# Performance work log

Hardware: AMD Instinct MI355X
Metric: run time of the kernel (lower is better)

## Reference

```python
import jax, jax.numpy as jnp
import numpy as np

N_NODES = 50000
N_EDGES = 800000
D = 128


def setup_inputs() -> dict:
    key = jax.random.key(0)
    ks = jax.random.split(key, 8)
    scale = 1.0 / np.sqrt(D)
    x = jax.random.normal(ks[0], (N_NODES, D), dtype=jnp.float32)
    edge_index = jax.random.randint(ks[1], (2, N_EDGES), 0, N_NODES, dtype=jnp.int64)
    return {
        "x": x,
        "edge_index": edge_index,
        "w1_l": jax.random.normal(ks[2], (D, D), dtype=jnp.float32) * scale,
        "w1_r": jax.random.normal(ks[3], (D, D), dtype=jnp.float32) * scale,
        "b1": jnp.zeros((D,), dtype=jnp.float32),
        "w2_l": jax.random.normal(ks[4], (D, D), dtype=jnp.float32) * scale,
        "w2_r": jax.random.normal(ks[5], (D, D), dtype=jnp.float32) * scale,
        "b2": jnp.zeros((D,), dtype=jnp.float32),
    }


def _sage_conv(x, src, dst, w_l, w_r, b):
    # mean aggregation of source features at destination nodes
    n = x.shape[0]
    msg = x[src]                                            # [E, D] gather
    agg = jax.ops.segment_sum(msg, dst, num_segments=n)      # [N, D] scatter-add
    cnt = jax.ops.segment_sum(jnp.ones((src.shape[0],), x.dtype), dst, num_segments=n)
    mean = agg / jnp.maximum(cnt, 1.0)[:, None]
    # out = lin_l(mean_agg) + lin_r(x) + bias  (PyG SAGEConv default)
    return mean @ w_l.T + x @ w_r.T + b


def reference(x, edge_index, w1_l, w1_r, b1, w2_l, w2_r, b2):
    src, dst = edge_index[0], edge_index[1]
    h = jax.nn.relu(_sage_conv(x, src, dst, w1_l, w1_r, b1))
    out = _sage_conv(h, src, dst, w2_l, w2_r, b2)
    return out
```

## Files before the change

### kernel.cpp

```cpp
#include <hip/hip_runtime.h>

#define D 128
#define CAP 48

typedef unsigned short u16;
typedef unsigned int u32;
typedef __attribute__((ext_vector_type(8))) short short8;
typedef __attribute__((ext_vector_type(4))) float f32x4;
typedef __attribute__((ext_vector_type(4))) unsigned short us4;
typedef __attribute__((ext_vector_type(8))) unsigned short us8;

__device__ __forceinline__ float bf2f(u16 v) {
    union { u32 u; float f; } c; c.u = ((u32)v) << 16; return c.f;
}
__device__ __forceinline__ u16 f2bf(float f) {
    union { float f; u32 u; } c; c.f = f;
    u32 r = (c.u + 0x7FFFu + ((c.u >> 16) & 1u)) >> 16;
    return (u16)r;
}

__global__ __launch_bounds__(256) void prep_kernel(const float* __restrict__ x,
                                                   u16* __restrict__ xb, int n8,
                                                   const float* __restrict__ w1l,
                                                   const float* __restrict__ w1r,
                                                   const float* __restrict__ w2l,
                                                   const float* __restrict__ w2r,
                                                   u16* __restrict__ wb1,
                                                   u16* __restrict__ wb2,
                                                   int* __restrict__ cnt, int Nceil,
                                                   int cvtBlocks, int wBlocks) {
    const int b = blockIdx.x;
    const int t = threadIdx.x;
    if (b < cvtBlocks) {
        int i = b * 256 + t;
        if (i < n8) {
            float4 v0 = reinterpret_cast<const float4*>(x)[2 * i];
            float4 v1 = reinterpret_cast<const float4*>(x)[2 * i + 1];
            us8 o;
            o[0] = f2bf(v0.x); o[1] = f2bf(v0.y); o[2] = f2bf(v0.z); o[3] = f2bf(v0.w);
            o[4] = f2bf(v1.x); o[5] = f2bf(v1.y); o[6] = f2bf(v1.z); o[7] = f2bf(v1.w);
            reinterpret_cast<us8*>(xb)[i] = o;
        }
    } else if (b < cvtBlocks + wBlocks) {
        int e = (b - cvtBlocks) * 256 + t;
        int which = e >> 15;
        int i = e & 32767;
        int j = i >> 8, k = i & 255;
        const float* wl = which ? w2l : w1l;
        const float* wr = which ? w2r : w1r;
        u16* wb = which ? wb2 : wb1;
        float v = (k < 128) ? wl[j * 128 + k] : wr[j * 128 + k - 128];
        wb[i] = f2bf(v);
    } else {
        int i = (b - cvtBlocks - wBlocks) * 256 + t;
        if (i < Nceil) cnt[i] = 0;
    }
}

__global__ __launch_bounds__(256) void fill_pad_xcd(const int* __restrict__ src,
                                                    const int* __restrict__ dst,
                                                    int* __restrict__ cnt,
                                                    int* __restrict__ edge_pad,
                                                    int E, int bucketDiv, int perChunk) {
    const int b = blockIdx.x & 7;
    const int chunk = blockIdx.x >> 3;
    const int lo = b * bucketDiv;
    const int hi = lo + bucketDiv;
    const int beg = chunk * perChunk;
    const int end = min(E, beg + perChunk);
    for (int base = beg + threadIdx.x * 4; base < end; base += 1024) {
        if (base + 3 < end) {
            int4 d = *reinterpret_cast<const int4*>(dst + base);
            if (d.x >= lo && d.x < hi) { int p = atomicAdd(&cnt[d.x], 1); if (p < CAP) edge_pad[d.x * CAP + p] = src[base + 0]; }
            if (d.y >= lo && d.y < hi) { int p = atomicAdd(&cnt[d.y], 1); if (p < CAP) edge_pad[d.y * CAP + p] = src[base + 1]; }
            if (d.z >= lo && d.z < hi) { int p = atomicAdd(&cnt[d.z], 1); if (p < CAP) edge_pad[d.z * CAP + p] = src[base + 2]; }
            if (d.w >= lo && d.w < hi) { int p = atomicAdd(&cnt[d.w], 1); if (p < CAP) edge_pad[d.w * CAP + p] = src[base + 3]; }
        } else {
            for (int j = 0; j < 4 && base + j < end; ++j) {
                int d = dst[base + j];
                if (d >= lo && d < hi) { int p = atomicAdd(&cnt[d], 1); if (p < CAP) edge_pad[d * CAP + p] = src[base + j]; }
            }
        }
    }
}

template <int RELU, int OUTBF16>
__global__ __launch_bounds__(256) void sage_fused(const u16* __restrict__ feat,
                                                  const int* __restrict__ cnt,
                                                  const int* __restrict__ edge_pad,
                                                  const u16* __restrict__ wb,
                                                  const float* __restrict__ bias,
                                                  float* __restrict__ outf,
                                                  u16* __restrict__ outb, int n) {
    __shared__ u16 sM[32 * 128];
    __shared__ int eLds[32 * CAP];
    __shared__ int degLds[32];
    const int t = threadIdx.x;
    const int base = blockIdx.x * 32;
    char* sMb = reinterpret_cast<char*>(sM);

    {
        const int4* gseg = reinterpret_cast<const int4*>(edge_pad + (size_t)base * CAP);
#pragma unroll
        for (int i = 0; i < (32 * CAP / 4 + 255) / 256; ++i) {
            int idx = i * 256 + t;
            if (idx < 32 * CAP / 4) reinterpret_cast<int4*>(eLds)[idx] = gseg[idx];
        }
        if (t < 32) degLds[t] = (base + t < n) ? cnt[base + t] : 0;
    }
    __syncthreads();

    {
        const int halfId = t >> 5;
        const int lane = t & 31;
#pragma unroll
        for (int rnd = 0; rnd < 4; ++rnd) {
            const int nl = rnd * 8 + halfId;
            const int deg = degLds[nl];
            const int stored = min(deg, CAP);
            const int* ep = &eLds[nl * CAP];

            float a0 = 0.f, a1 = 0.f, a2 = 0.f, a3 = 0.f;
            int j = 0;
            for (; j + 8 <= stored; j += 8) {
                int4 ia = *reinterpret_cast<const int4*>(ep + j);
                int4 ib = *reinterpret_cast<const int4*>(ep + j + 4);
                us4 v0 = *reinterpret_cast<const us4*>(feat + (size_t)ia.x * D + lane * 4);
                us4 v1 = *reinterpret_cast<const us4*>(feat + (size_t)ia.y * D + lane * 4);
                us4 v2 = *reinterpret_cast<const us4*>(feat + (size_t)ia.z * D + lane * 4);
                us4 v3 = *reinterpret_cast<const us4*>(feat + (size_t)ia.w * D + lane * 4);
                us4 v4 = *reinterpret_cast<const us4*>(feat + (size_t)ib.x * D + lane * 4);
                us4 v5 = *reinterpret_cast<const us4*>(feat + (size_t)ib.y * D + lane * 4);
                us4 v6 = *reinterpret_cast<const us4*>(feat + (size_t)ib.z * D + lane * 4);
                us4 v7 = *reinterpret_cast<const us4*>(feat + (size_t)ib.w * D + lane * 4);
                a0 += (bf2f(v0[0]) + bf2f(v1[0])) + (bf2f(v2[0]) + bf2f(v3[0]))
                    + (bf2f(v4[0]) + bf2f(v5[0])) + (bf2f(v6[0]) + bf2f(v7[0]));
                a1 += (bf2f(v0[1]) + bf2f(v1[1])) + (bf2f(v2[1]) + bf2f(v3[1]))
                    + (bf2f(v4[1]) + bf2f(v5[1])) + (bf2f(v6[1]) + bf2f(v7[1]));
                a2 += (bf2f(v0[2]) + bf2f(v1[2])) + (bf2f(v2[2]) + bf2f(v3[2]))
                    + (bf2f(v4[2]) + bf2f(v5[2])) + (bf2f(v6[2]) + bf2f(v7[2]));
                a3 += (bf2f(v0[3]) + bf2f(v1[3])) + (bf2f(v2[3]) + bf2f(v3[3]))
                    + (bf2f(v4[3]) + bf2f(v5[3])) + (bf2f(v6[3]) + bf2f(v7[3]));
            }
            for (; j < stored; ++j) {
                int s = ep[j];
                us4 v = *reinterpret_cast<const us4*>(feat + (size_t)s * D + lane * 4);
                a0 += bf2f(v[0]); a1 += bf2f(v[1]); a2 += bf2f(v[2]); a3 += bf2f(v[3]);
            }

            const float sc = (deg > 0) ? (1.f / (float)deg) : 0.f;
            us4 o;
            o[0] = f2bf(a0 * sc); o[1] = f2bf(a1 * sc); o[2] = f2bf(a2 * sc); o[3] = f2bf(a3 * sc);
            int lin = nl * 256 + lane * 8;
            *reinterpret_cast<us4*>(sMb + (lin ^ ((nl & 7) << 4))) = o;
        }
    }
    __syncthreads();

    const int wid = t >> 6, lane = t & 63;
    const int l15 = lane & 15, l4 = lane >> 4;
    const int colBase = wid * 32;

    int rowA[2];
#pragma unroll
    for (int m = 0; m < 2; ++m) {
        int r = base + m * 16 + l15;
        rowA[m] = (r < n) ? r : 0;
    }

    f32x4 acc[2][2];
#pragma unroll
    for (int m = 0; m < 2; ++m)
#pragma unroll
        for (int q = 0; q < 2; ++q) acc[m][q] = (f32x4){0.f, 0.f, 0.f, 0.f};

    const int swr = (l15 & 7) << 4;

#pragma unroll
    for (int ks = 0; ks < 8; ++ks) {
        short8 afr[2];
        if (ks < 4) {
#pragma unroll
            for (int m = 0; m < 2; ++m) {
                int lin = (m * 16 + l15) * 256 + ks * 64 + l4 * 16;
                afr[m] = *reinterpret_cast<const short8*>(sMb + (lin ^ swr));
            }
        } else {
            const int kk = (ks & 3) * 32 + l4 * 8;
#pragma unroll
            for (int m = 0; m < 2; ++m)
                afr[m] = *reinterpret_cast<const short8*>(feat + (size_t)rowA[m] * D + kk);
        }
#pragma unroll
        for (int q = 0; q < 2; ++q) {
            short8 bfr = *reinterpret_cast<const short8*>(
                wb + (size_t)(colBase + q * 16 + l15) * 256 + ks * 32 + l4 * 8);
#pragma unroll
            for (int m = 0; m < 2; ++m)
                acc[m][q] = __builtin_amdgcn_mfma_f32_16x16x32_bf16(afr[m], bfr, acc[m][q], 0, 0, 0);
        }
    }

#pragma unroll
    for (int q = 0; q < 2; ++q) {
        const int col = colBase + q * 16 + l15;
        const float bv = bias[col];
#pragma unroll
        for (int m = 0; m < 2; ++m) {
#pragma unroll
            for (int r = 0; r < 4; ++r) {
                int orow = base + m * 16 + l4 * 4 + r;
                if (orow < n) {
                    float v = acc[m][q][r] + bv;
                    if (RELU) v = fmaxf(v, 0.f);
                    if (OUTBF16)
                        outb[(size_t)orow * D + col] = f2bf(v);
                    else
                        outf[(size_t)orow * D + col] = v;
                }
            }
        }
    }
}

extern "C" void kernel_launch(void* const* d_in, const int* in_sizes, int n_in,
                              void* d_out, int out_size, void* d_ws, size_t ws_size,
                              hipStream_t stream) {
    const float* x   = (const float*)d_in[0];
    const int*   ei  = (const int*)d_in[1];
    const float* w1l = (const float*)d_in[2];
    const float* w1r = (const float*)d_in[3];
    const float* b1  = (const float*)d_in[4];
    const float* w2l = (const float*)d_in[5];
    const float* w2r = (const float*)d_in[6];
    const float* b2  = (const float*)d_in[7];
    float* out = (float*)d_out;

    const int N = in_sizes[0] / D;
    const int E = in_sizes[1] / 2;

    const int* src = ei;
    const int* dst = ei + E;

    const int gridFused = (N + 31) / 32;
    const int Nceil = gridFused * 32;

    char* ws = (char*)d_ws;
    auto align = [](size_t v) { return (v + 255) & ~(size_t)255; };
    const size_t featB = align((size_t)N * D * sizeof(u16));

    u16* xb       = (u16*)ws;   ws += featB;
    u16* hb       = (u16*)ws;   ws += featB;
    u16* wb1      = (u16*)ws;   ws += align(128 * 256 * sizeof(u16));
    u16* wb2      = (u16*)ws;   ws += align(128 * 256 * sizeof(u16));
    int* cnt      = (int*)ws;   ws += align((size_t)Nceil * sizeof(int));
    int* edge_pad = (int*)ws;   ws += align((size_t)Nceil * CAP * sizeof(int));

    const int n8        = N * D / 8;
    const int cvtBlocks = (n8 + 255) / 256;
    const int wBlocks   = 256;
    const int zBlocks   = (Nceil + 255) / 256;
    const int bucketDiv = (N + 7) / 8;
    const int perChunk  = 5120;
    const int chunks    = (E + perChunk - 1) / perChunk;

    prep_kernel<<<cvtBlocks + wBlocks + zBlocks, 256, 0, stream>>>(
        x, xb, n8, w1l, w1r, w2l, w2r, wb1, wb2, cnt, Nceil, cvtBlocks, wBlocks);

    fill_pad_xcd<<<8 * chunks, 256, 0, stream>>>(src, dst, cnt, edge_pad, E, bucketDiv, perChunk);

    sage_fused<1, 1><<<gridFused, 256, 0, stream>>>(xb, cnt, edge_pad, wb1, b1, nullptr, hb, N);

    sage_fused<0, 0><<<gridFused, 256, 0, stream>>>(hb, cnt, edge_pad, wb2, b2, out, nullptr, N);
}
```

Before: 145.5 us.

## Switch features to fp16 with packed half accumulation and 16-node tiles

Converts features and weights from bf16 to fp16 so the gather-sum can use packed half-precision vector adds instead of per-element bf16-to-float conversion and scalar float adds. It also widens the gather unroll to 16 neighbors, adds a 4-wide remainder loop, and halves the node tile to 16, so each block issues one MFMA row tile and the grid has twice as many blocks. Accumulating neighbor sums in fp16 loses precision and can overflow compared with float accumulation. The smaller tile also re-reads the weight matrix for every 16 nodes instead of every 32.

```diff
diff --git a/kernel.cpp b/kernel.cpp
--- a/kernel.cpp
+++ b/kernel.cpp
@@ -2,31 +2,23 @@
 
 #define D 128
 #define CAP 48
+#define TILE 16
 
 typedef unsigned short u16;
 typedef unsigned int u32;
-typedef __attribute__((ext_vector_type(8))) short short8;
+typedef _Float16 f16;
+typedef __attribute__((ext_vector_type(4))) _Float16 h4;
+typedef __attribute__((ext_vector_type(8))) _Float16 h8;
 typedef __attribute__((ext_vector_type(4))) float f32x4;
-typedef __attribute__((ext_vector_type(4))) unsigned short us4;
-typedef __attribute__((ext_vector_type(8))) unsigned short us8;
-
-__device__ __forceinline__ float bf2f(u16 v) {
-    union { u32 u; float f; } c; c.u = ((u32)v) << 16; return c.f;
-}
-__device__ __forceinline__ u16 f2bf(float f) {
-    union { float f; u32 u; } c; c.f = f;
-    u32 r = (c.u + 0x7FFFu + ((c.u >> 16) & 1u)) >> 16;
-    return (u16)r;
-}
 
 __global__ __launch_bounds__(256) void prep_kernel(const float* __restrict__ x,
-                                                   u16* __restrict__ xb, int n8,
+                                                   f16* __restrict__ xh, int n8,
                                                    const float* __restrict__ w1l,
                                                    const float* __restrict__ w1r,
                                                    const float* __restrict__ w2l,
                                                    const float* __restrict__ w2r,
-                                                   u16* __restrict__ wb1,
-                                                   u16* __restrict__ wb2,
+                                                   f16* __restrict__ wb1,
+                                                   f16* __restrict__ wb2,
                                                    int* __restrict__ cnt, int Nceil,
                                                    int cvtBlocks, int wBlocks) {
     const int b = blockIdx.x;
@@ -36,10 +28,10 @@
         if (i < n8) {
             float4 v0 = reinterpret_cast<const float4*>(x)[2 * i];
             float4 v1 = reinterpret_cast<const float4*>(x)[2 * i + 1];
-            us8 o;
-            o[0] = f2bf(v0.x); o[1] = f2bf(v0.y); o[2] = f2bf(v0.z); o[3] = f2bf(v0.w);
-            o[4] = f2bf(v1.x); o[5] = f2bf(v1.y); o[6] = f2bf(v1.z); o[7] = f2bf(v1.w);
-            reinterpret_cast<us8*>(xb)[i] = o;
+            h8 o;
+            o[0] = (f16)v0.x; o[1] = (f16)v0.y; o[2] = (f16)v0.z; o[3] = (f16)v0.w;
+            o[4] = (f16)v1.x; o[5] = (f16)v1.y; o[6] = (f16)v1.z; o[7] = (f16)v1.w;
+            reinterpret_cast<h8*>(xh)[i] = o;
         }
     } else if (b < cvtBlocks + wBlocks) {
         int e = (b - cvtBlocks) * 256 + t;
@@ -48,9 +40,9 @@
         int j = i >> 8, k = i & 255;
         const float* wl = which ? w2l : w1l;
         const float* wr = which ? w2r : w1r;
-        u16* wb = which ? wb2 : wb1;
+        f16* wb = which ? wb2 : wb1;
         float v = (k < 128) ? wl[j * 128 + k] : wr[j * 128 + k - 128];
-        wb[i] = f2bf(v);
+        wb[i] = (f16)v;
     } else {
         int i = (b - cvtBlocks - wBlocks) * 256 + t;
         if (i < Nceil) cnt[i] = 0;
@@ -84,29 +76,25 @@
     }
 }
 
-template <int RELU, int OUTBF16>
-__global__ __launch_bounds__(256) void sage_fused(const u16* __restrict__ feat,
+template <int RELU, int OUTF16>
+__global__ __launch_bounds__(256) void sage_fused(const f16* __restrict__ feat,
                                                   const int* __restrict__ cnt,
                                                   const int* __restrict__ edge_pad,
-                                                  const u16* __restrict__ wb,
+                                                  const f16* __restrict__ wb,
                                                   const float* __restrict__ bias,
                                                   float* __restrict__ outf,
-                                                  u16* __restrict__ outb, int n) {
-    __shared__ u16 sM[32 * 128];
-    __shared__ int eLds[32 * CAP];
-    __shared__ int degLds[32];
+                                                  f16* __restrict__ outh, int n) {
+    __shared__ f16 sM[TILE * 128];
+    __shared__ int eLds[TILE * CAP];
+    __shared__ int degLds[TILE];
     const int t = threadIdx.x;
-    const int base = blockIdx.x * 32;
+    const int base = blockIdx.x * TILE;
     char* sMb = reinterpret_cast<char*>(sM);
 
     {
         const int4* gseg = reinterpret_cast<const int4*>(edge_pad + (size_t)base * CAP);
-#pragma unroll
-        for (int i = 0; i < (32 * CAP / 4 + 255) / 256; ++i) {
-            int idx = i * 256 + t;
-            if (idx < 32 * CAP / 4) reinterpret_cast<int4*>(eLds)[idx] = gseg[idx];
-        }
-        if (t < 32) degLds[t] = (base + t < n) ? cnt[base + t] : 0;
+        if (t < TILE * CAP / 4) reinterpret_cast<int4*>(eLds)[t] = gseg[t];
+        if (t < TILE) degLds[t] = (base + t < n) ? cnt[base + t] : 0;
     }
     __syncthreads();
 
@@ -114,45 +102,55 @@
         const int halfId = t >> 5;
         const int lane = t & 31;
 #pragma unroll
-        for (int rnd = 0; rnd < 4; ++rnd) {
+        for (int rnd = 0; rnd < TILE / 8; ++rnd) {
             const int nl = rnd * 8 + halfId;
             const int deg = degLds[nl];
             const int stored = min(deg, CAP);
             const int* ep = &eLds[nl * CAP];
 
-            float a0 = 0.f, a1 = 0.f, a2 = 0.f, a3 = 0.f;
+            h4 acc = (h4){0, 0, 0, 0};
             int j = 0;
-            for (; j + 8 <= stored; j += 8) {
+            for (; j + 16 <= stored; j += 16) {
+                int4 i0 = *reinterpret_cast<const int4*>(ep + j);
+                int4 i1 = *reinterpret_cast<const int4*>(ep + j + 4);
+                int4 i2 = *reinterpret_cast<const int4*>(ep + j + 8);
+                int4 i3 = *reinterpret_cast<const int4*>(ep + j + 12);
+                h4 v0 = *reinterpret_cast<const h4*>(feat + (size_t)i0.x * D + lane * 4);
+                h4 v1 = *reinterpret_cast<const h4*>(feat + (size_t)i0.y * D + lane * 4);
+                h4 v2 = *reinterpret_cast<const h4*>(feat + (size_t)i0.z * D + lane * 4);
+                h4 v3 = *reinterpret_cast<const h4*>(feat + (size_t)i0.w * D + lane * 4);
+                h4 v4 = *reinterpret_cast<const h4*>(feat + (size_t)i1.x * D + lane * 4);
+                h4 v5 = *reinterpret_cast<const h4*>(feat + (size_t)i1.y * D + lane * 4);
+                h4 v6 = *reinterpret_cast<const h4*>(feat + (size_t)i1.z * D + lane * 4);
+                h4 v7 = *reinterpret_cast<const h4*>(feat + (size_t)i1.w * D + lane * 4);
+                h4 v8 = *reinterpret_cast<const h4*>(feat + (size_t)i2.x * D + lane * 4);
+                h4 v9 = *reinterpret_cast<const h4*>(feat + (size_t)i2.y * D + lane * 4);
+                h4 va = *reinterpret_cast<const h4*>(feat + (size_t)i2.z * D + lane * 4);
+                h4 vb = *reinterpret_cast<const h4*>(feat + (size_t)i2.w * D + lane * 4);
+                h4 vc = *reinterpret_cast<const h4*>(feat + (size_t)i3.x * D + lane * 4);
+                h4 vd = *reinterpret_cast<const h4*>(feat + (size_t)i3.y * D + lane * 4);
+                h4 ve = *reinterpret_cast<const h4*>(feat + (size_t)i3.z * D + lane * 4);
+                h4 vf = *reinterpret_cast<const h4*>(feat + (size_t)i3.w * D + lane * 4);
+                acc += ((v0 + v1) + (v2 + v3)) + ((v4 + v5) + (v6 + v7))
+                     + ((v8 + v9) + (va + vb)) + ((vc + vd) + (ve + vf));
+            }
+            for (; j + 4 <= stored; j += 4) {
                 int4 ia = *reinterpret_cast<const int4*>(ep + j);
-                int4 ib = *reinterpret_cast<const int4*>(ep + j + 4);
-                us4 v0 = *reinterpret_cast<const us4*>(feat + (size_t)ia.x * D + lane * 4);
-                us4 v1 = *reinterpret_cast<const us4*>(feat + (size_t)ia.y * D + lane * 4);
-                us4 v2 = *reinterpret_cast<const us4*>(feat + (size_t)ia.z * D + lane * 4);
-                us4 v3 = *reinterpret_cast<const us4*>(feat + (size_t)ia.w * D + lane * 4);
-                us4 v4 = *reinterpret_cast<const us4*>(feat + (size_t)ib.x * D + lane * 4);
-                us4 v5 = *reinterpret_cast<const us4*>(feat + (size_t)ib.y * D + lane * 4);
-                us4 v6 = *reinterpret_cast<const us4*>(feat + (size_t)ib.z * D + lane * 4);
-                us4 v7 = *reinterpret_cast<const us4*>(feat + (size_t)ib.w * D + lane * 4);
-                a0 += (bf2f(v0[0]) + bf2f(v1[0])) + (bf2f(v2[0]) + bf2f(v3[0]))
-                    + (bf2f(v4[0]) + bf2f(v5[0])) + (bf2f(v6[0]) + bf2f(v7[0]));
-                a1 += (bf2f(v0[1]) + bf2f(v1[1])) + (bf2f(v2[1]) + bf2f(v3[1]))
-                    + (bf2f(v4[1]) + bf2f(v5[1])) + (bf2f(v6[1]) + bf2f(v7[1]));
-                a2 += (bf2f(v0[2]) + bf2f(v1[2])) + (bf2f(v2[2]) + bf2f(v3[2]))
-                    + (bf2f(v4[2]) + bf2f(v5[2])) + (bf2f(v6[2]) + bf2f(v7[2]));
-                a3 += (bf2f(v0[3]) + bf2f(v1[3])) + (bf2f(v2[3]) + bf2f(v3[3]))
-                    + (bf2f(v4[3]) + bf2f(v5[3])) + (bf2f(v6[3]) + bf2f(v7[3]));
+                h4 v0 = *reinterpret_cast<const h4*>(feat + (size_t)ia.x * D + lane * 4);
+                h4 v1 = *reinterpret_cast<const h4*>(feat + (size_t)ia.y * D + lane * 4);
+                h4 v2 = *reinterpret_cast<const h4*>(feat + (size_t)ia.z * D + lane * 4);
+                h4 v3 = *reinterpret_cast<const h4*>(feat + (size_t)ia.w * D + lane * 4);
+                acc += (v0 + v1) + (v2 + v3);
             }
             for (; j < stored; ++j) {
                 int s = ep[j];
-                us4 v = *reinterpret_cast<const us4*>(feat + (size_t)s * D + lane * 4);
-                a0 += bf2f(v[0]); a1 += bf2f(v[1]); a2 += bf2f(v[2]); a3 += bf2f(v[3]);
-            }
-
-            const float sc = (deg > 0) ? (1.f / (float)deg) : 0.f;
-            us4 o;
-            o[0] = f2bf(a0 * sc); o[1] = f2bf(a1 * sc); o[2] = f2bf(a2 * sc); o[3] = f2bf(a3 * sc);
+                acc += *reinterpret_cast<const h4*>(feat + (size_t)s * D + lane * 4);
+            }
+
+            const f16 sc = (deg > 0) ? (f16)(1.f / (float)deg) : (f16)0;
+            h4 o = acc * (h4){sc, sc, sc, sc};
             int lin = nl * 256 + lane * 8;
-            *reinterpret_cast<us4*>(sMb + (lin ^ ((nl & 7) << 4))) = o;
+            *reinterpret_cast<h4*>(sMb + (lin ^ ((nl & 7) << 4))) = o;
         }
     }
     __syncthreads();
@@ -161,43 +159,30 @@
     const int l15 = lane & 15, l4 = lane >> 4;
     const int colBase = wid * 32;
 
-    int rowA[2];
-#pragma unroll
-    for (int m = 0; m < 2; ++m) {
-        int r = base + m * 16 + l15;
-        rowA[m] = (r < n) ? r : 0;
-    }
-
-    f32x4 acc[2][2];
-#pragma unroll
-    for (int m = 0; m < 2; ++m)
-#pragma unroll
-        for (int q = 0; q < 2; ++q) acc[m][q] = (f32x4){0.f, 0.f, 0.f, 0.f};
+    int rowA = base + l15;
+    if (rowA >= n) rowA = 0;
+
+    f32x4 acc0 = (f32x4){0.f, 0.f, 0.f, 0.f};
+    f32x4 acc1 = (f32x4){0.f, 0.f, 0.f, 0.f};
 
     const int swr = (l15 & 7) << 4;
 
 #pragma unroll
     for (int ks = 0; ks < 8; ++ks) {
-        short8 afr[2];
+        h8 afr;
         if (ks < 4) {
-#pragma unroll
-            for (int m = 0; m < 2; ++m) {
-                int lin = (m * 16 + l15) * 256 + ks * 64 + l4 * 16;
-                afr[m] = *reinterpret_cast<const short8*>(sMb + (lin ^ swr));
-            }
+            int lin = l15 * 256 + ks * 64 + l4 * 16;
+            afr = *reinterpret_cast<const h8*>(sMb + (lin ^ swr));
         } else {
             const int kk = (ks & 3) * 32 + l4 * 8;
-#pragma unroll
-            for (int m = 0; m < 2; ++m)
-                afr[m] = *reinterpret_cast<const short8*>(feat + (size_t)rowA[m] * D + kk);
+            afr = *reinterpret_cast<const h8*>(feat + (size_t)rowA * D + kk);
         }
 #pragma unroll
         for (int q = 0; q < 2; ++q) {
-            short8 bfr = *reinterpret_cast<const short8*>(
+            h8 bfr = *reinterpret_cast<const h8*>(
                 wb + (size_t)(colBase + q * 16 + l15) * 256 + ks * 32 + l4 * 8);
-#pragma unroll
-            for (int m = 0; m < 2; ++m)
-                acc[m][q] = __builtin_amdgcn_mfma_f32_16x16x32_bf16(afr[m], bfr, acc[m][q], 0, 0, 0);
+            f32x4& a = q ? acc1 : acc0;
+            a = __builtin_amdgcn_mfma_f32_16x16x32_f16(afr, bfr, a, 0, 0, 0);
         }
     }
 
@@ -205,19 +190,17 @@
     for (int q = 0; q < 2; ++q) {
         const int col = colBase + q * 16 + l15;
         const float bv = bias[col];
-#pragma unroll
-        for (int m = 0; m < 2; ++m) {
-#pragma unroll
-            for (int r = 0; r < 4; ++r) {
-                int orow = base + m * 16 + l4 * 4 + r;
-                if (orow < n) {
-                    float v = acc[m][q][r] + bv;
-                    if (RELU) v = fmaxf(v, 0.f);
-                    if (OUTBF16)
-                        outb[(size_t)orow * D + col] = f2bf(v);
-                    else
-                        outf[(size_t)orow * D + col] = v;
-                }
+        const f32x4& a = q ? acc1 : acc0;
+#pragma unroll
+        for (int r = 0; r < 4; ++r) {
+            int orow = base + l4 * 4 + r;
+            if (orow < n) {
+                float v = a[r] + bv;
+                if (RELU) v = fmaxf(v, 0.f);
+                if (OUTF16)
+                    outh[(size_t)orow * D + col] = (f16)v;
+                else
+                    outf[(size_t)orow * D + col] = v;
             }
         }
     }
@@ -242,17 +225,17 @@
     const int* src = ei;
     const int* dst = ei + E;
 
-    const int gridFused = (N + 31) / 32;
-    const int Nceil = gridFused * 32;
+    const int gridFused = (N + TILE - 1) / TILE;
+    const int Nceil = gridFused * TILE;
 
     char* ws = (char*)d_ws;
     auto align = [](size_t v) { return (v + 255) & ~(size_t)255; };
-    const size_t featB = align((size_t)N * D * sizeof(u16));
-
-    u16* xb       = (u16*)ws;   ws += featB;
-    u16* hb       = (u16*)ws;   ws += featB;
-    u16* wb1      = (u16*)ws;   ws += align(128 * 256 * sizeof(u16));
-    u16* wb2      = (u16*)ws;   ws += align(128 * 256 * sizeof(u16));
+    const size_t featB = align((size_t)N * D * sizeof(f16));
+
+    f16* xh       = (f16*)ws;   ws += featB;
+    f16* hh       = (f16*)ws;   ws += featB;
+    f16* wb1      = (f16*)ws;   ws += align(128 * 256 * sizeof(f16));
+    f16* wb2      = (f16*)ws;   ws += align(128 * 256 * sizeof(f16));
     int* cnt      = (int*)ws;   ws += align((size_t)Nceil * sizeof(int));
     int* edge_pad = (int*)ws;   ws += align((size_t)Nceil * CAP * sizeof(int));
 
@@ -265,11 +248,11 @@
     const int chunks    = (E + perChunk - 1) / perChunk;
 
     prep_kernel<<<cvtBlocks + wBlocks + zBlocks, 256, 0, stream>>>(
-        x, xb, n8, w1l, w1r, w2l, w2r, wb1, wb2, cnt, Nceil, cvtBlocks, wBlocks);
+        x, xh, n8, w1l, w1r, w2l, w2r, wb1, wb2, cnt, Nceil, cvtBlocks, wBlocks);
 
     fill_pad_xcd<<<8 * chunks, 256, 0, stream>>>(src, dst, cnt, edge_pad, E, bucketDiv, perChunk);
 
-    sage_fused<1, 1><<<gridFused, 256, 0, stream>>>(xb, cnt, edge_pad, wb1, b1, nullptr, hb, N);
-
-    sage_fused<0, 0><<<gridFused, 256, 0, stream>>>(hb, cnt, edge_pad, wb2, b2, out, nullptr, N);
-}
+    sage_fused<1, 1><<<gridFused, 256, 0, stream>>>(xh, cnt, edge_pad, wb1, b1, nullptr, hh, N);
+
+    sage_fused<0, 0><<<gridFused, 256, 0, stream>>>(hh, cnt, edge_pad, wb2, b2, out, nullptr, N);
+}
```

Result: slower. 170.3 us (+17.0%).
